# Kernel optimization log

Measured on AMD Instinct MI355X. Metric: run time of the kernel, lower is better.

Reference implementation:

```python
import jax, jax.numpy as jnp
import numpy as np

TEMPERATURE = 10000.0


def _grid_sample_bilinear(img, ix, iy):
    """torch.nn.functional.grid_sample equivalent (bilinear, zero padding,
    align_corners=False), with pixel coords ix, iy already unnormalized.
    img: [B,C,H,W]; ix, iy: [B,K,H,W]. Returns [B,C,K,H,W]."""
    B, C, H, W = img.shape
    K = ix.shape[1]
    x0 = jnp.floor(ix)
    y0 = jnp.floor(iy)
    x1 = x0 + 1.0
    y1 = y0 + 1.0
    wx1 = ix - x0
    wx0 = 1.0 - wx1
    wy1 = iy - y0
    wy0 = 1.0 - wy1
    flat = img.reshape(B, C, H * W)

    def corner(xc, yc, w):
        valid = (xc >= 0) & (xc <= W - 1) & (yc >= 0) & (yc <= H - 1)
        xi = jnp.clip(xc, 0, W - 1).astype(jnp.int32)
        yi = jnp.clip(yc, 0, H - 1).astype(jnp.int32)
        idx = (yi * W + xi).reshape(B, 1, -1)  # [B,1,K*H*W]
        g = jnp.take_along_axis(flat, jnp.broadcast_to(idx, (B, C, idx.shape[-1])), axis=2)
        g = g.reshape(B, C, K, H, W)
        wv = (w * valid.astype(img.dtype)).reshape(B, 1, K, H, W)
        return g * wv

    return (corner(x0, y0, wx0 * wy0) + corner(x1, y0, wx1 * wy0)
            + corner(x0, y1, wx0 * wy1) + corner(x1, y1, wx1 * wy1))


def _forward(left_features, right_features, offset_x, offset_y):
    B, C, H, W = left_features.shape
    dt = left_features.dtype
    # left coordinate grids (buffers built in __init__)
    lx = jnp.arange(W, dtype=dt)[None, None, None, :]               # [1,1,1,W]
    # faithful to original: y coords clamped to max = W-1 (no-op when H<=W)
    ly = jnp.clip(jnp.arange(H, dtype=dt), 0, W - 1)[None, None, :, None]  # [1,1,H,1]

    rx = jnp.clip(lx - offset_x, 0.0, W - 1.0)                      # [B,K,H,W]
    ry = jnp.clip(ly - offset_y, 0.0, H - 1.0)                      # [B,K,H,W]
    # normalize to [-1,1] as in original
    gx = (rx - W / 2) / (W / 2)
    gy = (ry - H / 2) / (H / 2)
    # unnormalize per align_corners=False convention
    ix = ((gx + 1.0) * W - 1.0) * 0.5
    iy = ((gy + 1.0) * H - 1.0) * 0.5

    sampled = _grid_sample_bilinear(right_features, ix, iy)         # [B,C,K,H,W]
    strength = jnp.mean(-jnp.abs(left_features[:, :, None] - sampled), axis=1) * TEMPERATURE  # [B,K,H,W]
    w = jax.nn.softmax(strength, axis=1)
    ox = jnp.sum(offset_x * w, axis=1, keepdims=True)               # [B,1,H,W]
    oy = jnp.sum(offset_y * w, axis=1, keepdims=True)               # [B,1,H,W]
    return ox, oy


def setup_inputs() -> dict:
    key = jax.random.key(0)
    k1, k2, k3, k4 = jax.random.split(key, 4)
    B, C, H, W, K = 1, 32, 256, 512, 10
    left_features = jax.random.normal(k1, (B, C, H, W), jnp.float32)
    right_features = jax.random.normal(k2, (B, C, H, W), jnp.float32)
    # horizontal disparity candidates in [0, 64) px; small vertical jitter
    offset_x = jax.random.uniform(k3, (B, K, H, W), jnp.float32) * 64.0
    offset_y = jax.random.normal(k4, (B, K, H, W), jnp.float32) * 2.0
    return {"left_features": left_features, "right_features": right_features,
            "offset_x": offset_x, "offset_y": offset_y}


def reference(left_features, right_features, offset_x, offset_y):
    return _forward(left_features, right_features, offset_x, offset_y)
```

## Files before the change

### kernel.cpp

```cpp
#include <hip/hip_runtime.h>

constexpr int C = 32, H = 256, W = 512, K = 10;
constexpr int HW = H * W;
constexpr float TEMP = 10000.0f;

__global__ __launch_bounds__(256) void transpose_chw_hwc(
    const float* __restrict__ in, float* __restrict__ out)
{
    __shared__ float t[C][257];
    const int base = blockIdx.x * 256;
    const int tid = threadIdx.x;
    #pragma unroll
    for (int c = 0; c < C; ++c)
        t[c][tid] = in[c * HW + base + tid];
    __syncthreads();
    #pragma unroll
    for (int j = 0; j < C; ++j) {
        int idx = j * 256 + tid;
        out[base * C + idx] = t[idx & 31][idx >> 5];
    }
}

__global__ __launch_bounds__(256) void disp_kernel_hwc(
    const float* __restrict__ lhwc, const float* __restrict__ rhwc,
    const float* __restrict__ offx, const float* __restrict__ offy,
    float* __restrict__ out)
{
    const int tid = threadIdx.x;
    const int q = tid & 3;
    const int p = blockIdx.x * 64 + (tid >> 2);
    const int w = p & (W - 1);
    const int h = p >> 9;

    const float4* lp = (const float4*)(lhwc + p * C + q * 8);
    float4 l0 = lp[0], l1 = lp[1];
    float lf[8] = {l0.x, l0.y, l0.z, l0.w, l1.x, l1.y, l1.z, l1.w};

    const float lx = (float)w;
    const float ly = (float)h;

    float s[K], okx[K], oky[K];

    #pragma unroll
    for (int k = 0; k < K; ++k) {
        const float ox = offx[k * HW + p];
        const float oy = offy[k * HW + p];
        okx[k] = ox; oky[k] = oy;

        float rx = fminf(fmaxf(lx - ox, 0.0f), (float)(W - 1));
        float ry = fminf(fmaxf(ly - oy, 0.0f), (float)(H - 1));
        float gx = (rx - (float)(W / 2)) / (float)(W / 2);
        float gy = (ry - (float)(H / 2)) / (float)(H / 2);
        float ix = ((gx + 1.0f) * (float)W - 1.0f) * 0.5f;
        float iy = ((gy + 1.0f) * (float)H - 1.0f) * 0.5f;

        float x0f = floorf(ix), y0f = floorf(iy);
        float wx1 = ix - x0f, wy1 = iy - y0f;
        float wx0 = 1.0f - wx1, wy0 = 1.0f - wy1;
        int x0 = (int)x0f, y0 = (int)y0f;
        int x1 = x0 + 1,  y1 = y0 + 1;

        float vx0 = (x0 >= 0 && x0 <= W - 1) ? 1.0f : 0.0f;
        float vx1 = (x1 >= 0 && x1 <= W - 1) ? 1.0f : 0.0f;
        float vy0 = (y0 >= 0 && y0 <= H - 1) ? 1.0f : 0.0f;
        float vy1 = (y1 >= 0 && y1 <= H - 1) ? 1.0f : 0.0f;
        float w00 = wx0 * wy0 * vx0 * vy0;
        float w01 = wx1 * wy0 * vx1 * vy0;
        float w10 = wx0 * wy1 * vx0 * vy1;
        float w11 = wx1 * wy1 * vx0 * vy1;
        w11 = wx1 * wy1 * vx1 * vy1;

        int xi0 = min(max(x0, 0), W - 1), xi1 = min(max(x1, 0), W - 1);
        int yi0 = min(max(y0, 0), H - 1), yi1 = min(max(y1, 0), H - 1);

        const float4* c00 = (const float4*)(rhwc + (yi0 * W + xi0) * C + q * 8);
        const float4* c01 = (const float4*)(rhwc + (yi0 * W + xi1) * C + q * 8);
        const float4* c10 = (const float4*)(rhwc + (yi1 * W + xi0) * C + q * 8);
        const float4* c11 = (const float4*)(rhwc + (yi1 * W + xi1) * C + q * 8);
        float4 a0 = c00[0], a1 = c00[1];
        float4 b0 = c01[0], b1 = c01[1];
        float4 d0 = c10[0], d1 = c10[1];
        float4 e0 = c11[0], e1 = c11[1];
        float ca[8] = {a0.x, a0.y, a0.z, a0.w, a1.x, a1.y, a1.z, a1.w};
        float cb[8] = {b0.x, b0.y, b0.z, b0.w, b1.x, b1.y, b1.z, b1.w};
        float cd[8] = {d0.x, d0.y, d0.z, d0.w, d1.x, d1.y, d1.z, d1.w};
        float ce[8] = {e0.x, e0.y, e0.z, e0.w, e1.x, e1.y, e1.z, e1.w};

        float acc = 0.0f;
        #pragma unroll
        for (int j = 0; j < 8; ++j) {
            float g = w00 * ca[j] + w01 * cb[j] + w10 * cd[j] + w11 * ce[j];
            acc += fabsf(lf[j] - g);
        }
        acc += __shfl_xor(acc, 1);
        acc += __shfl_xor(acc, 2);
        s[k] = acc * (-TEMP / (float)C);
    }

    float m = s[0];
    #pragma unroll
    for (int k = 1; k < K; ++k) m = fmaxf(m, s[k]);
    float den = 0.0f, sx = 0.0f, sy = 0.0f;
    #pragma unroll
    for (int k = 0; k < K; ++k) {
        float e = __expf(s[k] - m);
        den += e;
        sx += okx[k] * e;
        sy += oky[k] * e;
    }
    float inv = 1.0f / den;
    if (q == 0) {
        out[p]      = sx * inv;
        out[HW + p] = sy * inv;
    }
}

__global__ __launch_bounds__(256) void disp_kernel_chw(
    const float* __restrict__ left, const float* __restrict__ right,
    const float* __restrict__ offx, const float* __restrict__ offy,
    float* __restrict__ out)
{
    const int p = blockIdx.x * 256 + threadIdx.x;
    const int w = p & (W - 1);
    const int h = p >> 9;
    float lf[C];
    #pragma unroll
    for (int c = 0; c < C; ++c) lf[c] = left[c * HW + p];
    const float lx = (float)w, ly = (float)h;
    float s[K], okx[K], oky[K];
    #pragma unroll
    for (int k = 0; k < K; ++k) {
        const float ox = offx[k * HW + p], oy = offy[k * HW + p];
        okx[k] = ox; oky[k] = oy;
        float rx = fminf(fmaxf(lx - ox, 0.0f), (float)(W - 1));
        float ry = fminf(fmaxf(ly - oy, 0.0f), (float)(H - 1));
        float gx = (rx - 256.0f) / 256.0f, gy = (ry - 128.0f) / 128.0f;
        float ix = ((gx + 1.0f) * (float)W - 1.0f) * 0.5f;
        float iy = ((gy + 1.0f) * (float)H - 1.0f) * 0.5f;
        float x0f = floorf(ix), y0f = floorf(iy);
        float wx1 = ix - x0f, wy1 = iy - y0f;
        float wx0 = 1.0f - wx1, wy0 = 1.0f - wy1;
        int x0 = (int)x0f, y0 = (int)y0f, x1 = x0 + 1, y1 = y0 + 1;
        float vx0 = (x0 >= 0 && x0 <= W - 1) ? 1.0f : 0.0f;
        float vx1 = (x1 >= 0 && x1 <= W - 1) ? 1.0f : 0.0f;
        float vy0 = (y0 >= 0 && y0 <= H - 1) ? 1.0f : 0.0f;
        float vy1 = (y1 >= 0 && y1 <= H - 1) ? 1.0f : 0.0f;
        float w00 = wx0 * wy0 * vx0 * vy0, w01 = wx1 * wy0 * vx1 * vy0;
        float w10 = wx0 * wy1 * vx0 * vy1, w11 = wx1 * wy1 * vx1 * vy1;
        int xi0 = min(max(x0, 0), W - 1), xi1 = min(max(x1, 0), W - 1);
        int yi0 = min(max(y0, 0), H - 1), yi1 = min(max(y1, 0), H - 1);
        int i00 = yi0 * W + xi0, i01 = yi0 * W + xi1;
        int i10 = yi1 * W + xi0, i11 = yi1 * W + xi1;
        float acc = 0.0f;
        #pragma unroll
        for (int c = 0; c < C; ++c) {
            const float* rc = right + c * HW;
            acc += fabsf(lf[c] - (w00 * rc[i00] + w01 * rc[i01]
                                + w10 * rc[i10] + w11 * rc[i11]));
        }
        s[k] = acc * (-TEMP / (float)C);
    }
    float m = s[0];
    #pragma unroll
    for (int k = 1; k < K; ++k) m = fmaxf(m, s[k]);
    float den = 0.0f, sx = 0.0f, sy = 0.0f;
    #pragma unroll
    for (int k = 0; k < K; ++k) {
        float e = __expf(s[k] - m);
        den += e; sx += okx[k] * e; sy += oky[k] * e;
    }
    float inv = 1.0f / den;
    out[p] = sx * inv;
    out[HW + p] = sy * inv;
}

extern "C" void kernel_launch(void* const* d_in, const int* in_sizes, int n_in,
                              void* d_out, int out_size, void* d_ws, size_t ws_size,
                              hipStream_t stream) {
    const float* left  = (const float*)d_in[0];
    const float* right = (const float*)d_in[1];
    const float* offx  = (const float*)d_in[2];
    const float* offy  = (const float*)d_in[3];
    float* out = (float*)d_out;

    const size_t need = (size_t)2 * HW * C * sizeof(float);
    if (ws_size >= need) {
        float* rhwc = (float*)d_ws;
        float* lhwc = rhwc + (size_t)HW * C;
        transpose_chw_hwc<<<HW / 256, 256, 0, stream>>>(right, rhwc);
        transpose_chw_hwc<<<HW / 256, 256, 0, stream>>>(left,  lhwc);
        disp_kernel_hwc<<<HW / 64, 256, 0, stream>>>(lhwc, rhwc, offx, offy, out);
    } else {
        disp_kernel_chw<<<HW / 256, 256, 0, stream>>>(left, right, offx, offy, out);
    }
}
```

Before: 131.6 us.

## Drop left-feature transpose and read left directly from CHW layout

Removes the transpose of the left features. The disparity kernel now reads left values straight from the CHW layout, so one kernel launch and a full write-and-read round trip of a 16 MB tensor are gone. The right transpose now handles 128 pixels per block with 16 strided iterations, and all offsets are prefetched before the main loop. The main kernel also gets a min-blocks-per-SM launch bound. The CHW left reads are strided per thread (q*8+j channels), which may coalesce less well than the old vector loads.

```diff
diff --git a/kernel.cpp b/kernel.cpp
--- a/kernel.cpp
+++ b/kernel.cpp
@@ -4,25 +4,29 @@
 constexpr int HW = H * W;
 constexpr float TEMP = 10000.0f;
 
-__global__ __launch_bounds__(256) void transpose_chw_hwc(
+__global__ __launch_bounds__(256) void conv_right_hwc(
     const float* __restrict__ in, float* __restrict__ out)
 {
-    __shared__ float t[C][257];
-    const int base = blockIdx.x * 256;
+    __shared__ float t[C][129];
+    const int base = blockIdx.x * 128;
     const int tid = threadIdx.x;
     #pragma unroll
-    for (int c = 0; c < C; ++c)
-        t[c][tid] = in[c * HW + base + tid];
+    for (int i = 0; i < 16; ++i) {
+        int lin = i * 256 + tid;
+        int c = lin >> 7, px = lin & 127;
+        t[c][px] = in[c * HW + base + px];
+    }
     __syncthreads();
     #pragma unroll
-    for (int j = 0; j < C; ++j) {
-        int idx = j * 256 + tid;
-        out[base * C + idx] = t[idx & 31][idx >> 5];
-    }
-}
-
-__global__ __launch_bounds__(256) void disp_kernel_hwc(
-    const float* __restrict__ lhwc, const float* __restrict__ rhwc,
+    for (int i = 0; i < 16; ++i) {
+        int lin = i * 256 + tid;
+        int px = lin >> 5, c = lin & 31;
+        out[(base + px) * C + c] = t[c][px];
+    }
+}
+
+__global__ __launch_bounds__(256, 4) void disp_kernel_hwc(
+    const float* __restrict__ lchw, const float* __restrict__ rhwc,
     const float* __restrict__ offx, const float* __restrict__ offy,
     float* __restrict__ out)
 {
@@ -32,20 +36,27 @@
     const int w = p & (W - 1);
     const int h = p >> 9;
 
-    const float4* lp = (const float4*)(lhwc + p * C + q * 8);
-    float4 l0 = lp[0], l1 = lp[1];
-    float lf[8] = {l0.x, l0.y, l0.z, l0.w, l1.x, l1.y, l1.z, l1.w};
+    float lf[8];
+    #pragma unroll
+    for (int j = 0; j < 8; ++j) lf[j] = lchw[(q * 8 + j) * HW + p];
+
+    float okx[K], oky[K];
+    #pragma unroll
+    for (int k = 0; k < K; ++k) {
+        okx[k] = offx[k * HW + p];
+        oky[k] = offy[k * HW + p];
+    }
 
     const float lx = (float)w;
     const float ly = (float)h;
-
-    float s[K], okx[K], oky[K];
-
-    #pragma unroll
-    for (int k = 0; k < K; ++k) {
-        const float ox = offx[k * HW + p];
-        const float oy = offy[k * HW + p];
-        okx[k] = ox; oky[k] = oy;
+    const float4* rbase = (const float4*)rhwc;
+
+    float s[K];
+
+    #pragma unroll
+    for (int k = 0; k < K; ++k) {
+        const float ox = okx[k];
+        const float oy = oky[k];
 
         float rx = fminf(fmaxf(lx - ox, 0.0f), (float)(W - 1));
         float ry = fminf(fmaxf(ly - oy, 0.0f), (float)(H - 1));
@@ -67,20 +78,19 @@
         float w00 = wx0 * wy0 * vx0 * vy0;
         float w01 = wx1 * wy0 * vx1 * vy0;
         float w10 = wx0 * wy1 * vx0 * vy1;
-        float w11 = wx1 * wy1 * vx0 * vy1;
-        w11 = wx1 * wy1 * vx1 * vy1;
+        float w11 = wx1 * wy1 * vx1 * vy1;
 
         int xi0 = min(max(x0, 0), W - 1), xi1 = min(max(x1, 0), W - 1);
         int yi0 = min(max(y0, 0), H - 1), yi1 = min(max(y1, 0), H - 1);
 
-        const float4* c00 = (const float4*)(rhwc + (yi0 * W + xi0) * C + q * 8);
-        const float4* c01 = (const float4*)(rhwc + (yi0 * W + xi1) * C + q * 8);
-        const float4* c10 = (const float4*)(rhwc + (yi1 * W + xi0) * C + q * 8);
-        const float4* c11 = (const float4*)(rhwc + (yi1 * W + xi1) * C + q * 8);
-        float4 a0 = c00[0], a1 = c00[1];
-        float4 b0 = c01[0], b1 = c01[1];
-        float4 d0 = c10[0], d1 = c10[1];
-        float4 e0 = c11[0], e1 = c11[1];
+        int i00 = (yi0 * W + xi0) * 8 + q * 2;
+        int i01 = (yi0 * W + xi1) * 8 + q * 2;
+        int i10 = (yi1 * W + xi0) * 8 + q * 2;
+        int i11 = (yi1 * W + xi1) * 8 + q * 2;
+        float4 a0 = rbase[i00], a1 = rbase[i00 + 1];
+        float4 b0 = rbase[i01], b1 = rbase[i01 + 1];
+        float4 d0 = rbase[i10], d1 = rbase[i10 + 1];
+        float4 e0 = rbase[i11], e1 = rbase[i11 + 1];
         float ca[8] = {a0.x, a0.y, a0.z, a0.w, a1.x, a1.y, a1.z, a1.w};
         float cb[8] = {b0.x, b0.y, b0.z, b0.w, b1.x, b1.y, b1.z, b1.w};
         float cd[8] = {d0.x, d0.y, d0.z, d0.w, d1.x, d1.y, d1.z, d1.w};
@@ -183,13 +193,11 @@
     const float* offy  = (const float*)d_in[3];
     float* out = (float*)d_out;
 
-    const size_t need = (size_t)2 * HW * C * sizeof(float);
+    const size_t need = (size_t)HW * C * sizeof(float);
     if (ws_size >= need) {
         float* rhwc = (float*)d_ws;
-        float* lhwc = rhwc + (size_t)HW * C;
-        transpose_chw_hwc<<<HW / 256, 256, 0, stream>>>(right, rhwc);
-        transpose_chw_hwc<<<HW / 256, 256, 0, stream>>>(left,  lhwc);
-        disp_kernel_hwc<<<HW / 64, 256, 0, stream>>>(lhwc, rhwc, offx, offy, out);
+        conv_right_hwc<<<HW / 128, 256, 0, stream>>>(right, rhwc);
+        disp_kernel_hwc<<<HW / 64, 256, 0, stream>>>(left, rhwc, offx, offy, out);
     } else {
         disp_kernel_chw<<<HW / 256, 256, 0, stream>>>(left, right, offx, offy, out);
     }
```

Result: faster. 120.8 us (-8.2%).
